# Kernel optimization log

Hardware: AMD Instinct MI355X
Metric: run time of the kernel (lower is better)

## Reference

```python
import jax, jax.numpy as jnp
import numpy as np

H = 64  # hidden_dim


def _gru_cell(x, h, W_ih, W_hh, b_ih, b_hh):
    # PyTorch GRU gate order: reset (r), update (z), new (n)
    gx = x @ W_ih.T + b_ih            # [B, 3H]
    gh = h @ W_hh.T + b_hh            # [B, 3H]
    xr, xz, xn = jnp.split(gx, 3, axis=-1)
    hr, hz, hn = jnp.split(gh, 3, axis=-1)
    r = jax.nn.sigmoid(xr + hr)
    z = jax.nn.sigmoid(xz + hz)
    n = jnp.tanh(xn + r * hn)
    return (1.0 - z) * n + z * h


def setup_inputs() -> dict:
    key = jax.random.key(0)
    ks = jax.random.split(key, 11)
    B, T, F_in, A = 1024, 512, 128, 18
    s = 0.05
    return {
        "state": jax.random.normal(ks[0], (B, T, F_in), dtype=jnp.float32),
        "W_ih_l0": jax.random.normal(ks[1], (3 * H, F_in), dtype=jnp.float32) * s,
        "W_hh_l0": jax.random.normal(ks[2], (3 * H, H), dtype=jnp.float32) * s,
        "b_ih_l0": jax.random.normal(ks[3], (3 * H,), dtype=jnp.float32) * s,
        "b_hh_l0": jax.random.normal(ks[4], (3 * H,), dtype=jnp.float32) * s,
        "W_ih_l1": jax.random.normal(ks[5], (3 * H, H), dtype=jnp.float32) * s,
        "W_hh_l1": jax.random.normal(ks[6], (3 * H, H), dtype=jnp.float32) * s,
        "b_ih_l1": jax.random.normal(ks[7], (3 * H,), dtype=jnp.float32) * s,
        "b_hh_l1": jax.random.normal(ks[8], (3 * H,), dtype=jnp.float32) * s,
        "fc3_w": jax.random.normal(ks[9], (A, H), dtype=jnp.float32) * s,
        "fc3_b": jax.random.normal(ks[10], (A,), dtype=jnp.float32) * s,
    }


def reference(state, W_ih_l0, W_hh_l0, b_ih_l0, b_hh_l0,
              W_ih_l1, W_hh_l1, b_ih_l1, b_hh_l1, fc3_w, fc3_b):
    B = state.shape[0]
    h0 = jnp.zeros((B, H), dtype=state.dtype)
    h1 = jnp.zeros((B, H), dtype=state.dtype)
    xs = jnp.swapaxes(state, 0, 1)  # [T, B, F]

    def step(carry, x_t):
        h0, h1 = carry
        h0 = _gru_cell(x_t, h0, W_ih_l0, W_hh_l0, b_ih_l0, b_hh_l0)
        h1 = _gru_cell(h0, h1, W_ih_l1, W_hh_l1, b_ih_l1, b_hh_l1)
        return (h0, h1), None

    (_, h1_last), _ = jax.lax.scan(step, (h0, h1), xs)
    # out[:, -1] of the top GRU layer == final h1; then relu -> linear
    actions = jax.nn.relu(h1_last) @ fc3_w.T + fc3_b
    return actions
```

## Files before the change

kernel.cpp:

```cpp
#include <hip/hip_runtime.h>


#define Tn 512
#define Fn 128
#define Hn 64
#define An 18
#define TS 8
#define GX_T_ELEMS (64 * 4 * 3 * 64 * 4)
#define GX_BYTES ((size_t)Tn * GX_T_ELEMS * 2)

typedef _Float16 half8 __attribute__((ext_vector_type(8)));
typedef _Float16 half4 __attribute__((ext_vector_type(4)));
typedef float f32x4 __attribute__((ext_vector_type(4)));

#define MFMA(a, b, c) __builtin_amdgcn_mfma_f32_16x16x32_f16((a), (b), (c), 0, 0, 0)

static __device__ __forceinline__ float sigm(float x) {
    return __builtin_amdgcn_rcpf(1.0f + __builtin_amdgcn_exp2f(-1.4426950408889634f * x));
}
static __device__ __forceinline__ float tanh_f(float x) {
    return 2.0f * __builtin_amdgcn_rcpf(1.0f + __builtin_amdgcn_exp2f(-2.8853900817779268f * x)) - 1.0f;
}

__global__ __launch_bounds__(256, 1) void gx_pregemm(
    const float* __restrict__ state, const float* __restrict__ Wih0,
    const float* __restrict__ bih0, const float* __restrict__ bhh0,
    _Float16* __restrict__ gx)
{
    const int tid = threadIdx.x;
    const int wv = tid >> 6, lane = tid & 63;
    const int c = lane & 15, q = lane >> 4;
    const int tile = blockIdx.x;
    const int t0 = blockIdx.y * TS;

    half8 Bx[3][4];
    f32x4 binit[3];
#pragma unroll
    for (int gsel = 0; gsel < 3; ++gsel) {
        const int g = gsel * 64 + wv * 16 + c;
        const float b = bih0[g] + (gsel < 2 ? bhh0[g] : 0.0f);
        binit[gsel] = (f32x4){b, b, b, b};
#pragma unroll
        for (int ks = 0; ks < 4; ++ks) {
            const float* p = Wih0 + g * Fn + ks * 32 + q * 8;
#pragma unroll
            for (int j = 0; j < 8; ++j) Bx[gsel][ks][j] = (_Float16)p[j];
        }
    }
    const float* srow = state + (size_t)(tile * 16 + c) * (Tn * Fn) + (size_t)t0 * Fn;
    _Float16* gp = gx + (size_t)t0 * GX_T_ELEMS + tile * 3072 + wv * 768 + lane * 4;

    for (int j = 0; j < TS; ++j) {
        half8 xf[4];
#pragma unroll
        for (int ks = 0; ks < 4; ++ks) {
            f32x4 a  = *(const f32x4*)(srow + (size_t)j * Fn + ks * 32 + q * 8);
            f32x4 b2 = *(const f32x4*)(srow + (size_t)j * Fn + ks * 32 + q * 8 + 4);
#pragma unroll
            for (int i = 0; i < 4; ++i) { xf[ks][i] = (_Float16)a[i]; xf[ks][4 + i] = (_Float16)b2[i]; }
        }
        f32x4 a0 = binit[0], a1 = binit[1], a2 = binit[2];
#pragma unroll
        for (int ks = 0; ks < 4; ++ks) {
            a0 = MFMA(xf[ks], Bx[0][ks], a0);
            a1 = MFMA(xf[ks], Bx[1][ks], a1);
            a2 = MFMA(xf[ks], Bx[2][ks], a2);
        }
        half4 o0, o1, o2;
#pragma unroll
        for (int i = 0; i < 4; ++i) {
            o0[i] = (_Float16)a0[i]; o1[i] = (_Float16)a1[i]; o2[i] = (_Float16)a2[i];
        }
        *(half4*)(gp + (size_t)j * GX_T_ELEMS)       = o0;
        *(half4*)(gp + (size_t)j * GX_T_ELEMS + 256) = o1;
        *(half4*)(gp + (size_t)j * GX_T_ELEMS + 512) = o2;
    }
}

template <bool PRE>
__global__ __launch_bounds__(512, 1) void gru_rec(
    const float* __restrict__ state, const _Float16* __restrict__ gx,
    const float* __restrict__ Wih0, const float* __restrict__ Whh0,
    const float* __restrict__ bih0, const float* __restrict__ bhh0,
    const float* __restrict__ Wih1, const float* __restrict__ Whh1,
    const float* __restrict__ bih1, const float* __restrict__ bhh1,
    const float* __restrict__ fcw, const float* __restrict__ fcb,
    float* __restrict__ out)
{
    const int tid = threadIdx.x;
    const int wv8 = tid >> 6;
    const int lane = tid & 63, c = lane & 15, q = lane >> 4;
    const bool isL0 = (wv8 < 4);
    const int wv = wv8 & 3;
    const int tile = blockIdx.x, r0 = tile * 16;
    const int gc = wv * 16 + c;

    __shared__ __align__(16) _Float16 h0buf[2][16 * 80];
    __shared__ __align__(16) _Float16 h1buf[2][16 * 80];
    __shared__ float fbuf[16 * 64];

    for (int i = tid; i < 2 * 16 * 80; i += 512) {
        (&h0buf[0][0])[i] = (_Float16)0.0f;
        (&h1buf[0][0])[i] = (_Float16)0.0f;
    }

    half8 BA[3][2], BB[3][2], BX[3][4];
    f32x4 bias_r, bias_z, bias_xn, bias_hn;
    if (isL0) {
#pragma unroll
        for (int gsel = 0; gsel < 3; ++gsel) {
            const int g = gsel * 64 + gc;
#pragma unroll
            for (int ks = 0; ks < 2; ++ks) {
                const float* p = Whh0 + g * Hn + ks * 32 + q * 8;
#pragma unroll
                for (int j = 0; j < 8; ++j) BA[gsel][ks][j] = (_Float16)p[j];
            }
            if (!PRE) {
#pragma unroll
                for (int ks = 0; ks < 4; ++ks) {
                    const float* p = Wih0 + g * Fn + ks * 32 + q * 8;
#pragma unroll
                    for (int j = 0; j < 8; ++j) BX[gsel][ks][j] = (_Float16)p[j];
                }
            }
        }
        const float br = bih0[gc] + bhh0[gc];
        const float bz = bih0[64 + gc] + bhh0[64 + gc];
        const float bxn = bih0[128 + gc];
        const float bhn = bhh0[128 + gc];
        bias_r  = (f32x4){br, br, br, br};
        bias_z  = (f32x4){bz, bz, bz, bz};
        bias_xn = (f32x4){bxn, bxn, bxn, bxn};
        bias_hn = (f32x4){bhn, bhn, bhn, bhn};
    } else {
#pragma unroll
        for (int gsel = 0; gsel < 3; ++gsel) {
            const int g = gsel * 64 + gc;
#pragma unroll
            for (int ks = 0; ks < 2; ++ks) {
                const float* pa = Wih1 + g * Hn + ks * 32 + q * 8;
                const float* pb = Whh1 + g * Hn + ks * 32 + q * 8;
#pragma unroll
                for (int j = 0; j < 8; ++j) {
                    BA[gsel][ks][j] = (_Float16)pa[j];
                    BB[gsel][ks][j] = (_Float16)pb[j];
                }
            }
        }
        const float br = bih1[gc] + bhh1[gc];
        const float bz = bih1[64 + gc] + bhh1[64 + gc];
        const float bxn = bih1[128 + gc];
        const float bhn = bhh1[128 + gc];
        bias_r  = (f32x4){br, br, br, br};
        bias_z  = (f32x4){bz, bz, bz, bz};
        bias_xn = (f32x4){bxn, bxn, bxn, bxn};
        bias_hn = (f32x4){bhn, bhn, bhn, bhn};
    }

    const _Float16* gp = gx + tile * 3072 + wv * 768 + lane * 4;
    half4 g0p, g1p, g2p;
    const float* srow = state + (size_t)(r0 + c) * (Tn * Fn);
    f32x4 xp[8];
    if (isL0) {
        if (PRE) {
            g0p = *(const half4*)(gp);
            g1p = *(const half4*)(gp + 256);
            g2p = *(const half4*)(gp + 512);
            gp += GX_T_ELEMS;
        } else {
#pragma unroll
            for (int ks = 0; ks < 4; ++ks) {
                xp[2 * ks]     = *(const f32x4*)(srow + ks * 32 + q * 8);
                xp[2 * ks + 1] = *(const f32x4*)(srow + ks * 32 + q * 8 + 4);
            }
        }
    }

    f32x4 hreg = (f32x4){0.f, 0.f, 0.f, 0.f};
    const int ardr = c * 80 + q * 8;
    const int wrow = (q * 4) * 80 + gc;

    for (int t = 0; t <= Tn; ++t) {
        __syncthreads();
        const int pr = (t & 1) ^ 1, pw = (t & 1);
        if (isL0) {
            if (t < Tn) {
                f32x4 accr, accz, accxn, acchn;
                if (PRE) {
#pragma unroll
                    for (int i = 0; i < 4; ++i) {
                        accr[i]  = (float)g0p[i];
                        accz[i]  = (float)g1p[i];
                        accxn[i] = (float)g2p[i];
                    }
                    if (t + 1 < Tn) {
                        g0p = *(const half4*)(gp);
                        g1p = *(const half4*)(gp + 256);
                        g2p = *(const half4*)(gp + 512);
                        gp += GX_T_ELEMS;
                    }
                } else {
                    half8 xf[4];
#pragma unroll
                    for (int ks = 0; ks < 4; ++ks) {
#pragma unroll
                        for (int i = 0; i < 4; ++i) {
                            xf[ks][i]     = (_Float16)xp[2 * ks][i];
                            xf[ks][4 + i] = (_Float16)xp[2 * ks + 1][i];
                        }
                    }
                    const int tnx = (t + 1 < Tn) ? (t + 1) : t;
#pragma unroll
                    for (int ks = 0; ks < 4; ++ks) {
                        xp[2 * ks]     = *(const f32x4*)(srow + (size_t)tnx * Fn + ks * 32 + q * 8);
                        xp[2 * ks + 1] = *(const f32x4*)(srow + (size_t)tnx * Fn + ks * 32 + q * 8 + 4);
                    }
                    accr = bias_r; accz = bias_z; accxn = bias_xn;
#pragma unroll
                    for (int ks = 0; ks < 4; ++ks) {
                        accr  = MFMA(xf[ks], BX[0][ks], accr);
                        accz  = MFMA(xf[ks], BX[1][ks], accz);
                        accxn = MFMA(xf[ks], BX[2][ks], accxn);
                    }
                }
                const half8 hf0 = *(const half8*)&h0buf[pr][ardr];
                const half8 hf1 = *(const half8*)&h0buf[pr][ardr + 32];
                accr  = MFMA(hf0, BA[0][0], accr);
                accr  = MFMA(hf1, BA[0][1], accr);
                accz  = MFMA(hf0, BA[1][0], accz);
                accz  = MFMA(hf1, BA[1][1], accz);
                acchn = MFMA(hf0, BA[2][0], bias_hn);
                acchn = MFMA(hf1, BA[2][1], acchn);
#pragma unroll
                for (int i = 0; i < 4; ++i) {
                    const float rg = sigm(accr[i]);
                    const float zg = sigm(accz[i]);
                    const float ng = tanh_f(accxn[i] + rg * acchn[i]);
                    hreg[i] = ng + zg * (hreg[i] - ng);
                }
#pragma unroll
                for (int i = 0; i < 4; ++i) h0buf[pw][wrow + i * 80] = (_Float16)hreg[i];
            }
        } else {
            if (t >= 1) {
                const half8 xf0 = *(const half8*)&h0buf[pr][ardr];
                const half8 xf1 = *(const half8*)&h0buf[pr][ardr + 32];
                const half8 hf0 = *(const half8*)&h1buf[pw][ardr];
                const half8 hf1 = *(const half8*)&h1buf[pw][ardr + 32];
                f32x4 accr = bias_r, accz = bias_z, accxn = bias_xn, acchn;
                accr  = MFMA(xf0, BA[0][0], accr);
                accr  = MFMA(xf1, BA[0][1], accr);
                accz  = MFMA(xf0, BA[1][0], accz);
                accz  = MFMA(xf1, BA[1][1], accz);
                accxn = MFMA(xf0, BA[2][0], accxn);
                accxn = MFMA(xf1, BA[2][1], accxn);
                accr  = MFMA(hf0, BB[0][0], accr);
                accr  = MFMA(hf1, BB[0][1], accr);
                accz  = MFMA(hf0, BB[1][0], accz);
                accz  = MFMA(hf1, BB[1][1], accz);
                acchn = MFMA(hf0, BB[2][0], bias_hn);
                acchn = MFMA(hf1, BB[2][1], acchn);
#pragma unroll
                for (int i = 0; i < 4; ++i) {
                    const float rg = sigm(accr[i]);
                    const float zg = sigm(accz[i]);
                    const float ng = tanh_f(accxn[i] + rg * acchn[i]);
                    hreg[i] = ng + zg * (hreg[i] - ng);
                }
#pragma unroll
                for (int i = 0; i < 4; ++i) h1buf[pr][wrow + i * 80] = (_Float16)hreg[i];
            }
        }
    }

    if (!isL0) {
#pragma unroll
        for (int i = 0; i < 4; ++i) fbuf[(q * 4 + i) * 64 + gc] = fmaxf(hreg[i], 0.0f);
    }
    __syncthreads();
    for (int idx = tid; idx < 16 * An; idx += 512) {
        const int row = idx / An, a = idx - row * An;
        float acc = fcb[a];
#pragma unroll 16
        for (int k = 0; k < Hn; ++k) acc += fbuf[row * 64 + k] * fcw[a * Hn + k];
        out[(size_t)(r0 + row) * An + a] = acc;
    }
}

extern "C" void kernel_launch(void* const* d_in, const int* in_sizes, int n_in,
                              void* d_out, int out_size, void* d_ws, size_t ws_size,
                              hipStream_t stream) {
    const float* state = (const float*)d_in[0];
    const float* Wih0  = (const float*)d_in[1];
    const float* Whh0  = (const float*)d_in[2];
    const float* bih0  = (const float*)d_in[3];
    const float* bhh0  = (const float*)d_in[4];
    const float* Wih1  = (const float*)d_in[5];
    const float* Whh1  = (const float*)d_in[6];
    const float* bih1  = (const float*)d_in[7];
    const float* bhh1  = (const float*)d_in[8];
    const float* fcw   = (const float*)d_in[9];
    const float* fcb   = (const float*)d_in[10];
    float* out = (float*)d_out;

    if (ws_size >= GX_BYTES) {
        _Float16* gx = (_Float16*)d_ws;
        gx_pregemm<<<dim3(64, Tn / TS), 256, 0, stream>>>(state, Wih0, bih0, bhh0, gx);
        gru_rec<true><<<64, 512, 0, stream>>>(state, gx, Wih0, Whh0, bih0, bhh0,
                                              Wih1, Whh1, bih1, bhh1, fcw, fcb, out);
    } else {
        gru_rec<false><<<64, 512, 0, stream>>>(state, (const _Float16*)d_ws,
                                               Wih0, Whh0, bih0, bhh0,
                                               Wih1, Whh1, bih1, bhh1, fcw, fcb, out);
    }
}
```

Before: 816.8 us.

## Fuse input projection into recurrent kernel via producer wavefronts and LDS ring

Drops the separate pre-GEMM kernel and its global fp16 workspace. A third group of four wavefronts computes the layer-0 input projection one step ahead and passes it through a double-buffered fp32 LDS ring. The layer-0 recurrent wavefronts then run only the hidden-state MFMAs on the critical path. Block size grows to 768 threads and the LDS row stride changes from 80 to 72, which may alter bank conflicts and adds more waves to each barrier.

```diff
diff --git a/kernel.cpp b/kernel.cpp
--- a/kernel.cpp
+++ b/kernel.cpp
@@ -5,12 +5,9 @@
 #define Fn 128
 #define Hn 64
 #define An 18
-#define TS 8
-#define GX_T_ELEMS (64 * 4 * 3 * 64 * 4)
-#define GX_BYTES ((size_t)Tn * GX_T_ELEMS * 2)
+#define HS 72
 
 typedef _Float16 half8 __attribute__((ext_vector_type(8)));
-typedef _Float16 half4 __attribute__((ext_vector_type(4)));
 typedef float f32x4 __attribute__((ext_vector_type(4)));
 
 #define MFMA(a, b, c) __builtin_amdgcn_mfma_f32_16x16x32_f16((a), (b), (c), 0, 0, 0)
@@ -22,64 +19,8 @@
     return 2.0f * __builtin_amdgcn_rcpf(1.0f + __builtin_amdgcn_exp2f(-2.8853900817779268f * x)) - 1.0f;
 }
 
-__global__ __launch_bounds__(256, 1) void gx_pregemm(
-    const float* __restrict__ state, const float* __restrict__ Wih0,
-    const float* __restrict__ bih0, const float* __restrict__ bhh0,
-    _Float16* __restrict__ gx)
-{
-    const int tid = threadIdx.x;
-    const int wv = tid >> 6, lane = tid & 63;
-    const int c = lane & 15, q = lane >> 4;
-    const int tile = blockIdx.x;
-    const int t0 = blockIdx.y * TS;
-
-    half8 Bx[3][4];
-    f32x4 binit[3];
-#pragma unroll
-    for (int gsel = 0; gsel < 3; ++gsel) {
-        const int g = gsel * 64 + wv * 16 + c;
-        const float b = bih0[g] + (gsel < 2 ? bhh0[g] : 0.0f);
-        binit[gsel] = (f32x4){b, b, b, b};
-#pragma unroll
-        for (int ks = 0; ks < 4; ++ks) {
-            const float* p = Wih0 + g * Fn + ks * 32 + q * 8;
-#pragma unroll
-            for (int j = 0; j < 8; ++j) Bx[gsel][ks][j] = (_Float16)p[j];
-        }
-    }
-    const float* srow = state + (size_t)(tile * 16 + c) * (Tn * Fn) + (size_t)t0 * Fn;
-    _Float16* gp = gx + (size_t)t0 * GX_T_ELEMS + tile * 3072 + wv * 768 + lane * 4;
-
-    for (int j = 0; j < TS; ++j) {
-        half8 xf[4];
-#pragma unroll
-        for (int ks = 0; ks < 4; ++ks) {
-            f32x4 a  = *(const f32x4*)(srow + (size_t)j * Fn + ks * 32 + q * 8);
-            f32x4 b2 = *(const f32x4*)(srow + (size_t)j * Fn + ks * 32 + q * 8 + 4);
-#pragma unroll
-            for (int i = 0; i < 4; ++i) { xf[ks][i] = (_Float16)a[i]; xf[ks][4 + i] = (_Float16)b2[i]; }
-        }
-        f32x4 a0 = binit[0], a1 = binit[1], a2 = binit[2];
-#pragma unroll
-        for (int ks = 0; ks < 4; ++ks) {
-            a0 = MFMA(xf[ks], Bx[0][ks], a0);
-            a1 = MFMA(xf[ks], Bx[1][ks], a1);
-            a2 = MFMA(xf[ks], Bx[2][ks], a2);
-        }
-        half4 o0, o1, o2;
-#pragma unroll
-        for (int i = 0; i < 4; ++i) {
-            o0[i] = (_Float16)a0[i]; o1[i] = (_Float16)a1[i]; o2[i] = (_Float16)a2[i];
-        }
-        *(half4*)(gp + (size_t)j * GX_T_ELEMS)       = o0;
-        *(half4*)(gp + (size_t)j * GX_T_ELEMS + 256) = o1;
-        *(half4*)(gp + (size_t)j * GX_T_ELEMS + 512) = o2;
-    }
-}
-
-template <bool PRE>
-__global__ __launch_bounds__(512, 1) void gru_rec(
-    const float* __restrict__ state, const _Float16* __restrict__ gx,
+__global__ __launch_bounds__(768) void gru_fused(
+    const float* __restrict__ state,
     const float* __restrict__ Wih0, const float* __restrict__ Whh0,
     const float* __restrict__ bih0, const float* __restrict__ bhh0,
     const float* __restrict__ Wih1, const float* __restrict__ Whh1,
@@ -87,52 +28,90 @@
     const float* __restrict__ fcw, const float* __restrict__ fcb,
     float* __restrict__ out)
 {
-    const int tid = threadIdx.x;
-    const int wv8 = tid >> 6;
+    const int tid  = threadIdx.x;
+    const int wv12 = tid >> 6;
     const int lane = tid & 63, c = lane & 15, q = lane >> 4;
-    const bool isL0 = (wv8 < 4);
-    const int wv = wv8 & 3;
-    const int tile = blockIdx.x, r0 = tile * 16;
-    const int gc = wv * 16 + c;
-
-    __shared__ __align__(16) _Float16 h0buf[2][16 * 80];
-    __shared__ __align__(16) _Float16 h1buf[2][16 * 80];
+    const int wv   = wv12 & 3;
+    const int r0   = blockIdx.x * 16;
+    const int gc   = wv * 16 + c;
+    const int role = (wv12 < 4) ? 0 : (wv12 < 8 ? 1 : 2);
+
+    __shared__ __align__(16) float    gxring[2][4][3][64][4];
+    __shared__ __align__(16) _Float16 h0buf[2][16 * HS];
+    __shared__ __align__(16) _Float16 h1buf[2][16 * HS];
     __shared__ float fbuf[16 * 64];
 
-    for (int i = tid; i < 2 * 16 * 80; i += 512) {
+    for (int i = tid; i < 2 * 16 * HS; i += 768) {
         (&h0buf[0][0])[i] = (_Float16)0.0f;
         (&h1buf[0][0])[i] = (_Float16)0.0f;
     }
 
-    half8 BA[3][2], BB[3][2], BX[3][4];
-    f32x4 bias_r, bias_z, bias_xn, bias_hn;
-    if (isL0) {
+    half8 W[12];
+    f32x4 bias0, bias1, bias2, bias3;
+    f32x4 xf32[8];
+    f32x4 hreg = {0.f, 0.f, 0.f, 0.f};
+    const float* srow = state + (size_t)(r0 + c) * (Tn * Fn);
+
+    if (role == 0) {
 #pragma unroll
         for (int gsel = 0; gsel < 3; ++gsel) {
             const int g = gsel * 64 + gc;
 #pragma unroll
+            for (int ks = 0; ks < 4; ++ks) {
+                const float* p = Wih0 + g * Fn + ks * 32 + q * 8;
+#pragma unroll
+                for (int j = 0; j < 8; ++j) W[gsel * 4 + ks][j] = (_Float16)p[j];
+            }
+        }
+        {
+            const float b0 = bih0[gc] + bhh0[gc];
+            const float b1 = bih0[64 + gc] + bhh0[64 + gc];
+            const float b2 = bih0[128 + gc];
+            bias0 = (f32x4){b0, b0, b0, b0};
+            bias1 = (f32x4){b1, b1, b1, b1};
+            bias2 = (f32x4){b2, b2, b2, b2};
+        }
+#pragma unroll
+        for (int ks = 0; ks < 4; ++ks) {
+            xf32[2 * ks]     = *(const f32x4*)(srow + ks * 32 + q * 8);
+            xf32[2 * ks + 1] = *(const f32x4*)(srow + ks * 32 + q * 8 + 4);
+        }
+        half8 xf[4];
+#pragma unroll
+        for (int ks = 0; ks < 4; ++ks)
+#pragma unroll
+            for (int i = 0; i < 4; ++i) {
+                xf[ks][i]     = (_Float16)xf32[2 * ks][i];
+                xf[ks][4 + i] = (_Float16)xf32[2 * ks + 1][i];
+            }
+        f32x4 a0 = bias0, a1 = bias1, a2 = bias2;
+#pragma unroll
+        for (int ks = 0; ks < 4; ++ks) {
+            a0 = MFMA(xf[ks], W[ks], a0);
+            a1 = MFMA(xf[ks], W[4 + ks], a1);
+            a2 = MFMA(xf[ks], W[8 + ks], a2);
+        }
+        *(f32x4*)&gxring[0][wv][0][lane][0] = a0;
+        *(f32x4*)&gxring[0][wv][1][lane][0] = a1;
+        *(f32x4*)&gxring[0][wv][2][lane][0] = a2;
+#pragma unroll
+        for (int ks = 0; ks < 4; ++ks) {
+            xf32[2 * ks]     = *(const f32x4*)(srow + Fn + ks * 32 + q * 8);
+            xf32[2 * ks + 1] = *(const f32x4*)(srow + Fn + ks * 32 + q * 8 + 4);
+        }
+    } else if (role == 1) {
+#pragma unroll
+        for (int gsel = 0; gsel < 3; ++gsel) {
+            const int g = gsel * 64 + gc;
+#pragma unroll
             for (int ks = 0; ks < 2; ++ks) {
                 const float* p = Whh0 + g * Hn + ks * 32 + q * 8;
 #pragma unroll
-                for (int j = 0; j < 8; ++j) BA[gsel][ks][j] = (_Float16)p[j];
-            }
-            if (!PRE) {
-#pragma unroll
-                for (int ks = 0; ks < 4; ++ks) {
-                    const float* p = Wih0 + g * Fn + ks * 32 + q * 8;
-#pragma unroll
-                    for (int j = 0; j < 8; ++j) BX[gsel][ks][j] = (_Float16)p[j];
-                }
-            }
-        }
-        const float br = bih0[gc] + bhh0[gc];
-        const float bz = bih0[64 + gc] + bhh0[64 + gc];
-        const float bxn = bih0[128 + gc];
+                for (int j = 0; j < 8; ++j) W[gsel * 2 + ks][j] = (_Float16)p[j];
+            }
+        }
         const float bhn = bhh0[128 + gc];
-        bias_r  = (f32x4){br, br, br, br};
-        bias_z  = (f32x4){bz, bz, bz, bz};
-        bias_xn = (f32x4){bxn, bxn, bxn, bxn};
-        bias_hn = (f32x4){bhn, bhn, bhn, bhn};
+        bias3 = (f32x4){bhn, bhn, bhn, bhn};
     } else {
 #pragma unroll
         for (int gsel = 0; gsel < 3; ++gsel) {
@@ -143,8 +122,8 @@
                 const float* pb = Whh1 + g * Hn + ks * 32 + q * 8;
 #pragma unroll
                 for (int j = 0; j < 8; ++j) {
-                    BA[gsel][ks][j] = (_Float16)pa[j];
-                    BB[gsel][ks][j] = (_Float16)pb[j];
+                    W[gsel * 2 + ks][j]     = (_Float16)pa[j];
+                    W[6 + gsel * 2 + ks][j] = (_Float16)pb[j];
                 }
             }
         }
@@ -152,86 +131,59 @@
         const float bz = bih1[64 + gc] + bhh1[64 + gc];
         const float bxn = bih1[128 + gc];
         const float bhn = bhh1[128 + gc];
-        bias_r  = (f32x4){br, br, br, br};
-        bias_z  = (f32x4){bz, bz, bz, bz};
-        bias_xn = (f32x4){bxn, bxn, bxn, bxn};
-        bias_hn = (f32x4){bhn, bhn, bhn, bhn};
-    }
-
-    const _Float16* gp = gx + tile * 3072 + wv * 768 + lane * 4;
-    half4 g0p, g1p, g2p;
-    const float* srow = state + (size_t)(r0 + c) * (Tn * Fn);
-    f32x4 xp[8];
-    if (isL0) {
-        if (PRE) {
-            g0p = *(const half4*)(gp);
-            g1p = *(const half4*)(gp + 256);
-            g2p = *(const half4*)(gp + 512);
-            gp += GX_T_ELEMS;
-        } else {
-#pragma unroll
-            for (int ks = 0; ks < 4; ++ks) {
-                xp[2 * ks]     = *(const f32x4*)(srow + ks * 32 + q * 8);
-                xp[2 * ks + 1] = *(const f32x4*)(srow + ks * 32 + q * 8 + 4);
-            }
-        }
-    }
-
-    f32x4 hreg = (f32x4){0.f, 0.f, 0.f, 0.f};
-    const int ardr = c * 80 + q * 8;
-    const int wrow = (q * 4) * 80 + gc;
+        bias0 = (f32x4){br, br, br, br};
+        bias1 = (f32x4){bz, bz, bz, bz};
+        bias2 = (f32x4){bxn, bxn, bxn, bxn};
+        bias3 = (f32x4){bhn, bhn, bhn, bhn};
+    }
+
+    const int ardr = c * HS + q * 8;
+    const int wrow = (q * 4) * HS + gc;
 
     for (int t = 0; t <= Tn; ++t) {
         __syncthreads();
-        const int pr = (t & 1) ^ 1, pw = (t & 1);
-        if (isL0) {
+        const int pr = (t & 1) ^ 1, pw = t & 1;
+        if (role == 0) {
+            if (t < Tn - 1) {
+                half8 xf[4];
+#pragma unroll
+                for (int ks = 0; ks < 4; ++ks)
+#pragma unroll
+                    for (int i = 0; i < 4; ++i) {
+                        xf[ks][i]     = (_Float16)xf32[2 * ks][i];
+                        xf[ks][4 + i] = (_Float16)xf32[2 * ks + 1][i];
+                    }
+                const int tnx = (t + 2 < Tn) ? (t + 2) : (Tn - 1);
+#pragma unroll
+                for (int ks = 0; ks < 4; ++ks) {
+                    xf32[2 * ks]     = *(const f32x4*)(srow + (size_t)tnx * Fn + ks * 32 + q * 8);
+                    xf32[2 * ks + 1] = *(const f32x4*)(srow + (size_t)tnx * Fn + ks * 32 + q * 8 + 4);
+                }
+                f32x4 a0 = bias0, a1 = bias1, a2 = bias2;
+#pragma unroll
+                for (int ks = 0; ks < 4; ++ks) {
+                    a0 = MFMA(xf[ks], W[ks], a0);
+                    a1 = MFMA(xf[ks], W[4 + ks], a1);
+                    a2 = MFMA(xf[ks], W[8 + ks], a2);
+                }
+                const int slot = (t + 1) & 1;
+                *(f32x4*)&gxring[slot][wv][0][lane][0] = a0;
+                *(f32x4*)&gxring[slot][wv][1][lane][0] = a1;
+                *(f32x4*)&gxring[slot][wv][2][lane][0] = a2;
+            }
+        } else if (role == 1) {
             if (t < Tn) {
-                f32x4 accr, accz, accxn, acchn;
-                if (PRE) {
-#pragma unroll
-                    for (int i = 0; i < 4; ++i) {
-                        accr[i]  = (float)g0p[i];
-                        accz[i]  = (float)g1p[i];
-                        accxn[i] = (float)g2p[i];
-                    }
-                    if (t + 1 < Tn) {
-                        g0p = *(const half4*)(gp);
-                        g1p = *(const half4*)(gp + 256);
-                        g2p = *(const half4*)(gp + 512);
-                        gp += GX_T_ELEMS;
-                    }
-                } else {
-                    half8 xf[4];
-#pragma unroll
-                    for (int ks = 0; ks < 4; ++ks) {
-#pragma unroll
-                        for (int i = 0; i < 4; ++i) {
-                            xf[ks][i]     = (_Float16)xp[2 * ks][i];
-                            xf[ks][4 + i] = (_Float16)xp[2 * ks + 1][i];
-                        }
-                    }
-                    const int tnx = (t + 1 < Tn) ? (t + 1) : t;
-#pragma unroll
-                    for (int ks = 0; ks < 4; ++ks) {
-                        xp[2 * ks]     = *(const f32x4*)(srow + (size_t)tnx * Fn + ks * 32 + q * 8);
-                        xp[2 * ks + 1] = *(const f32x4*)(srow + (size_t)tnx * Fn + ks * 32 + q * 8 + 4);
-                    }
-                    accr = bias_r; accz = bias_z; accxn = bias_xn;
-#pragma unroll
-                    for (int ks = 0; ks < 4; ++ks) {
-                        accr  = MFMA(xf[ks], BX[0][ks], accr);
-                        accz  = MFMA(xf[ks], BX[1][ks], accz);
-                        accxn = MFMA(xf[ks], BX[2][ks], accxn);
-                    }
-                }
+                f32x4 accr  = *(const f32x4*)&gxring[t & 1][wv][0][lane][0];
+                f32x4 accz  = *(const f32x4*)&gxring[t & 1][wv][1][lane][0];
+                f32x4 accxn = *(const f32x4*)&gxring[t & 1][wv][2][lane][0];
                 const half8 hf0 = *(const half8*)&h0buf[pr][ardr];
                 const half8 hf1 = *(const half8*)&h0buf[pr][ardr + 32];
-                accr  = MFMA(hf0, BA[0][0], accr);
-                accr  = MFMA(hf1, BA[0][1], accr);
-                accz  = MFMA(hf0, BA[1][0], accz);
-                accz  = MFMA(hf1, BA[1][1], accz);
-                acchn = MFMA(hf0, BA[2][0], bias_hn);
-                acchn = MFMA(hf1, BA[2][1], acchn);
+                accr = MFMA(hf0, W[0], accr);
+                accr = MFMA(hf1, W[1], accr);
+                accz = MFMA(hf0, W[2], accz);
+                accz = MFMA(hf1, W[3], accz);
+                f32x4 acchn = MFMA(hf0, W[4], bias3);
+                acchn = MFMA(hf1, W[5], acchn);
 #pragma unroll
                 for (int i = 0; i < 4; ++i) {
                     const float rg = sigm(accr[i]);
@@ -240,7 +192,7 @@
                     hreg[i] = ng + zg * (hreg[i] - ng);
                 }
 #pragma unroll
-                for (int i = 0; i < 4; ++i) h0buf[pw][wrow + i * 80] = (_Float16)hreg[i];
+                for (int i = 0; i < 4; ++i) h0buf[pw][wrow + i * HS] = (_Float16)hreg[i];
             }
         } else {
             if (t >= 1) {
@@ -248,19 +200,18 @@
                 const half8 xf1 = *(const half8*)&h0buf[pr][ardr + 32];
                 const half8 hf0 = *(const half8*)&h1buf[pw][ardr];
                 const half8 hf1 = *(const half8*)&h1buf[pw][ardr + 32];
-                f32x4 accr = bias_r, accz = bias_z, accxn = bias_xn, acchn;
-                accr  = MFMA(xf0, BA[0][0], accr);
-                accr  = MFMA(xf1, BA[0][1], accr);
-                accz  = MFMA(xf0, BA[1][0], accz);
-                accz  = MFMA(xf1, BA[1][1], accz);
-                accxn = MFMA(xf0, BA[2][0], accxn);
-                accxn = MFMA(xf1, BA[2][1], accxn);
-                accr  = MFMA(hf0, BB[0][0], accr);
-                accr  = MFMA(hf1, BB[0][1], accr);
-                accz  = MFMA(hf0, BB[1][0], accz);
-                accz  = MFMA(hf1, BB[1][1], accz);
-                acchn = MFMA(hf0, BB[2][0], bias_hn);
-                acchn = MFMA(hf1, BB[2][1], acchn);
+                f32x4 accr = MFMA(xf0, W[0], bias0);
+                accr = MFMA(xf1, W[1], accr);
+                f32x4 accz = MFMA(xf0, W[2], bias1);
+                accz = MFMA(xf1, W[3], accz);
+                f32x4 accxn = MFMA(xf0, W[4], bias2);
+                accxn = MFMA(xf1, W[5], accxn);
+                accr = MFMA(hf0, W[6], accr);
+                accr = MFMA(hf1, W[7], accr);
+                accz = MFMA(hf0, W[8], accz);
+                accz = MFMA(hf1, W[9], accz);
+                f32x4 acchn = MFMA(hf0, W[10], bias3);
+                acchn = MFMA(hf1, W[11], acchn);
 #pragma unroll
                 for (int i = 0; i < 4; ++i) {
                     const float rg = sigm(accr[i]);
@@ -269,17 +220,17 @@
                     hreg[i] = ng + zg * (hreg[i] - ng);
                 }
 #pragma unroll
-                for (int i = 0; i < 4; ++i) h1buf[pr][wrow + i * 80] = (_Float16)hreg[i];
-            }
-        }
-    }
-
-    if (!isL0) {
+                for (int i = 0; i < 4; ++i) h1buf[pr][wrow + i * HS] = (_Float16)hreg[i];
+            }
+        }
+    }
+
+    if (role == 2) {
 #pragma unroll
         for (int i = 0; i < 4; ++i) fbuf[(q * 4 + i) * 64 + gc] = fmaxf(hreg[i], 0.0f);
     }
     __syncthreads();
-    for (int idx = tid; idx < 16 * An; idx += 512) {
+    for (int idx = tid; idx < 16 * An; idx += 768) {
         const int row = idx / An, a = idx - row * An;
         float acc = fcb[a];
 #pragma unroll 16
@@ -304,14 +255,6 @@
     const float* fcb   = (const float*)d_in[10];
     float* out = (float*)d_out;
 
-    if (ws_size >= GX_BYTES) {
-        _Float16* gx = (_Float16*)d_ws;
-        gx_pregemm<<<dim3(64, Tn / TS), 256, 0, stream>>>(state, Wih0, bih0, bhh0, gx);
-        gru_rec<true><<<64, 512, 0, stream>>>(state, gx, Wih0, Whh0, bih0, bhh0,
-                                              Wih1, Whh1, bih1, bhh1, fcw, fcb, out);
-    } else {
-        gru_rec<false><<<64, 512, 0, stream>>>(state, (const _Float16*)d_ws,
-                                               Wih0, Whh0, bih0, bhh0,
-                                               Wih1, Whh1, bih1, bhh1, fcw, fcb, out);
-    }
-}
+    gru_fused<<<64, 768, 0, stream>>>(state, Wih0, Whh0, bih0, bhh0,
+                                      Wih1, Whh1, bih1, bhh1, fcw, fcb, out);
+}
```

After: 741.9 us. -9.2%, faster.
